# Kernel optimization log

Measured on AMD Instinct MI355X. Metric: run time of the kernel, lower is better.

The kernel has to match this reference:

```python
import jax, jax.numpy as jnp
from jax import lax
import numpy as np

# ChannelMamba (bimamba_type='v2') from Wave-MambaAD VSSBlock.
# Dims: b=4, d_model=256 (channel dim of u), h=w=64 -> l=h*w=4096=dim,
# expand=1 -> d_inner=256, d_state=16, dt_rank=ceil(256/16)=16.
B_, DM, H_, W_ = 4, 256, 64, 64
L_ = H_ * W_            # == init arg `dim` (LayerNorm + depthwise-conv channels)
DI = DM                 # d_inner = expand * d_model
N_ = 16                 # d_state
R_ = 16                 # dt_rank


def setup_inputs() -> dict:
    key = jax.random.key(0)
    ks = jax.random.split(key, 12)
    s = 0.05
    # dt_proj bias init exactly as in the module: inv-softplus of dt in [1e-3, 1e-1]
    rs = np.random.RandomState(0)
    dt = np.exp(rs.rand(DI) * (np.log(0.1) - np.log(0.001)) + np.log(0.001))
    dt = np.clip(dt, 1e-4, None)
    inv_dt = dt + np.log1p(-np.exp(-dt))
    A_log = jnp.log(jnp.tile(jnp.arange(1, N_ + 1, dtype=jnp.float32), (DI, 1)))
    return {
        "u": jax.random.normal(ks[0], (B_, DM, H_, W_), jnp.float32),
        "in_proj_w": jax.random.normal(ks[1], (2 * DI, DM), jnp.float32) * s,
        "conv_w": jax.random.normal(ks[2], (L_, 1, 3, 3), jnp.float32) * s,  # depthwise, groups=L_
        "conv_b": jnp.zeros((L_,), jnp.float32),
        "x_proj_w": jax.random.normal(ks[3], (R_ + 2 * N_, DI), jnp.float32) * s,
        "dt_proj_w": jax.random.normal(ks[4], (DI, R_), jnp.float32) * (R_ ** -0.5),
        "dt_bias": jnp.asarray(inv_dt, jnp.float32),
        "A_log": A_log,
        "D": jnp.ones((DI,), jnp.float32),
        "x_proj_b_w": jax.random.normal(ks[5], (R_ + 2 * N_, DI), jnp.float32) * s,
        "dt_proj_b_w": jax.random.normal(ks[6], (DI, R_), jnp.float32) * (R_ ** -0.5),
        "A_b_log": A_log,
        "D_b": jnp.ones((DI,), jnp.float32),
        "ln_w": jnp.ones((L_,), jnp.float32),
        "ln_b": jnp.zeros((L_,), jnp.float32),
        "ln1_w": jnp.ones((L_,), jnp.float32),
        "ln1_b": jnp.zeros((L_,), jnp.float32),
    }


def _layernorm(x, w, b, eps=1e-5):
    m = jnp.mean(x, axis=-1, keepdims=True)
    v = jnp.mean(jnp.square(x - m), axis=-1, keepdims=True)
    return (x - m) * lax.rsqrt(v + eps) * w + b


def _selective_scan(u, delta, A, Bm, Cm, D, z, delta_bias):
    # u, delta, z: (b,d,l); A: (d,n); Bm, Cm: (b,n,l); D, delta_bias: (d,)
    delta = jax.nn.softplus(delta + delta_bias[None, :, None])
    dT = jnp.transpose(delta, (2, 0, 1))  # (l,b,d)
    uT = jnp.transpose(u, (2, 0, 1))      # (l,b,d)
    BT = jnp.transpose(Bm, (2, 0, 1))     # (l,b,n)
    CT = jnp.transpose(Cm, (2, 0, 1))     # (l,b,n)

    def step(hcar, inp):
        d_t, u_t, B_t, C_t = inp
        dA = jnp.exp(d_t[:, :, None] * A)                       # (b,d,n)
        hcar = hcar * dA + (d_t * u_t)[:, :, None] * B_t[:, None, :]
        y_t = jnp.einsum('bdn,bn->bd', hcar, C_t)
        return hcar, y_t

    h0 = jnp.zeros((u.shape[0], u.shape[1], A.shape[1]), u.dtype)
    _, ys = lax.scan(step, h0, (dT, uT, BT, CT))                 # ys: (l,b,d)
    y = jnp.transpose(ys, (1, 2, 0)) + D[None, :, None] * u      # (b,d,l)
    return y * jax.nn.silu(z)                                    # internal z-gate of selective_scan_fn


def reference(u, in_proj_w, conv_w, conv_b, x_proj_w, dt_proj_w, dt_bias, A_log, D,
              x_proj_b_w, dt_proj_b_w, A_b_log, D_b, ln_w, ln_b, ln1_w, ln1_b):
    b, d, h, w = u.shape
    l = h * w
    r = dt_proj_w.shape[1]
    n = A_log.shape[1]
    u_bld = u.reshape(b, d, l).transpose(0, 2, 1)                # (b,l,d)
    xz = jnp.einsum('ed,bld->bel', in_proj_w, u_bld)             # (b,2*d_inner,l), no bias
    x, z = jnp.split(xz, 2, axis=1)                              # each (b,d_inner,l)

    # depthwise 3x3 conv: channels = l, spatial = (1, d_inner), padding 1 (no activation!)
    xc = x.transpose(0, 2, 1)[:, :, None, :]                     # (b,l,1,d_inner)
    xc = lax.conv_general_dilated(xc, conv_w, (1, 1), ((1, 1), (1, 1)),
                                  feature_group_count=l,
                                  dimension_numbers=('NCHW', 'OIHW', 'NCHW'))
    x = (xc + conv_b[None, :, None, None])[:, :, 0, :].transpose(0, 2, 1)  # (b,d_inner,l)

    def proj(xp_w, dtp_w):
        dbl = jnp.einsum('kd,bdl->bkl', xp_w, x)                 # (b,r+2n,l)
        dt = jnp.einsum('dr,brl->bdl', dtp_w, dbl[:, :r])        # (b,d_inner,l), no bias here
        return dt, dbl[:, r:r + n], dbl[:, r + n:]               # dt, B, C

    A = -jnp.exp(A_log)
    A_b = -jnp.exp(A_b_log)
    dt, Bm, Cm = proj(x_proj_w, dt_proj_w)
    dtb, Bb, Cb = proj(x_proj_b_w, dt_proj_b_w)

    y = _selective_scan(x, dt, A, Bm, Cm, D, z, dt_bias)
    # backward scan: flipped input; NOTE: module uses forward dt_bias and unflipped z here
    yb = _selective_scan(x[:, :, ::-1], dtb, A_b, Bb, Cb, D_b, z, dt_bias)

    out = _layernorm(y, ln_w, ln_b) * jax.nn.silu(z)
    out_b = _layernorm(yb, ln1_w, ln1_b) * jax.nn.silu(z)
    return (out + out_b[:, :, ::-1]).reshape(b, d, h, w)
```

## Files before the change

kernel.cpp:

```cpp
#include <hip/hip_runtime.h>
#include <math.h>

#define BN 4
#define DD 256
#define LL 4096
#define NS 16
#define NCH 128
#define CT 32
#define BROW 20
#define LOG2E 1.4426950408889634f

typedef __bf16 bf16x8 __attribute__((ext_vector_type(8)));
typedef float f32x4 __attribute__((ext_vector_type(4)));

__device__ __forceinline__ float softplus_f(float v) {
  float e = __builtin_amdgcn_exp2f(v * LOG2E);
  float r = 0.69314718056f * __builtin_amdgcn_logf(1.f + e);
  return v > 20.f ? v : r;
}
__device__ __forceinline__ float silu_f(float v) {
  return v / (1.f + __expf(-v));
}
__device__ __forceinline__ f32x4 exp2v(f32x4 a) {
  f32x4 r;
  r[0] = __builtin_amdgcn_exp2f(a[0]);
  r[1] = __builtin_amdgcn_exp2f(a[1]);
  r[2] = __builtin_amdgcn_exp2f(a[2]);
  r[3] = __builtin_amdgcn_exp2f(a[3]);
  return r;
}
__device__ __forceinline__ float quad_reduce(float v) {
  int t = __builtin_amdgcn_mov_dpp(__float_as_int(v), 0xB1, 0xF, 0xF, true);
  v += __int_as_float(t);
  t = __builtin_amdgcn_mov_dpp(__float_as_int(v), 0x4E, 0xF, 0xF, true);
  return v + __int_as_float(t);
}

__global__ __launch_bounds__(256) void k1_mfma(
    const float* __restrict__ W, const float* __restrict__ u,
    float* __restrict__ xpre, float* __restrict__ zb) {
  __shared__ float Af[128 * 36];
  __shared__ float Bf[32 * 68];
  const int l0 = blockIdx.x * 64;
  const int e0 = blockIdx.y * 128;
  const int b  = blockIdx.z;
  const int tid = threadIdx.x;
  const int lane = tid & 63, w = tid >> 6;
  const int m16 = lane & 15, quad = lane >> 4;

  f32x4 acc[2][4];
#pragma unroll
  for (int i = 0; i < 2; ++i)
#pragma unroll
    for (int j = 0; j < 4; ++j) acc[i][j] = (f32x4){0.f, 0.f, 0.f, 0.f};

  const float* Ub = u + (size_t)b * DD * LL;

  for (int k0 = 0; k0 < DD; k0 += 32) {
    if (k0) __syncthreads();
#pragma unroll
    for (int it = 0; it < 4; ++it) {
      int f4 = tid + it * 256;
      int e = f4 >> 3, kq = f4 & 7;
      *(float4*)&Af[e * 36 + kq * 4] =
          *(const float4*)(W + (size_t)(e0 + e) * DD + k0 + kq * 4);
    }
#pragma unroll
    for (int it = 0; it < 2; ++it) {
      int f4 = tid + it * 256;
      int kk = f4 >> 4, lq = f4 & 15;
      *(float4*)&Bf[kk * 68 + lq * 4] =
          *(const float4*)(Ub + (size_t)(k0 + kk) * LL + l0 + lq * 4);
    }
    __syncthreads();
    bf16x8 afr[2], bfr[4];
#pragma unroll
    for (int te = 0; te < 2; ++te) {
      const float* src = &Af[(w * 32 + te * 16 + m16) * 36 + quad * 8];
      bf16x8 t;
#pragma unroll
      for (int j = 0; j < 8; ++j) t[j] = (__bf16)src[j];
      afr[te] = t;
    }
#pragma unroll
    for (int tl = 0; tl < 4; ++tl) {
      bf16x8 t;
#pragma unroll
      for (int j = 0; j < 8; ++j) t[j] = (__bf16)Bf[(quad * 8 + j) * 68 + tl * 16 + m16];
      bfr[tl] = t;
    }
#pragma unroll
    for (int te = 0; te < 2; ++te)
#pragma unroll
      for (int tl = 0; tl < 4; ++tl)
        acc[te][tl] = __builtin_amdgcn_mfma_f32_16x16x32_bf16(afr[te], bfr[tl], acc[te][tl], 0, 0, 0);
  }

#pragma unroll
  for (int te = 0; te < 2; ++te) {
#pragma unroll
    for (int tl = 0; tl < 4; ++tl) {
      int col = l0 + tl * 16 + m16;
#pragma unroll
      for (int r = 0; r < 4; ++r) {
        int e = e0 + w * 32 + te * 16 + quad * 4 + r;
        float v = acc[te][tl][r];
        if (e < DD) xpre[((size_t)b * DD + e) * LL + col] = v;
        else        zb[((size_t)b * DD + (e - DD)) * LL + col] = v;
      }
    }
  }
}

__global__ __launch_bounds__(256) void k2_conv(
    const float* __restrict__ xpre, const float* __restrict__ cw,
    const float* __restrict__ cb, float* __restrict__ xo) {
  const int bd = blockIdx.x;
  const int d = bd & 255;
  const size_t row = (size_t)bd * LL;
  const float* r1 = xpre + row;
  const bool has0 = d > 0, has2 = d < DD - 1;
  for (int j = threadIdx.x; j < LL; j += 256) {
    float w0 = cw[j * 9 + 3], w1 = cw[j * 9 + 4], w2 = cw[j * 9 + 5];
    float v = cb[j] + r1[j] * w1;
    if (has0) v += r1[j - LL] * w0;
    if (has2) v += r1[j + LL] * w2;
    xo[row + j] = v;
  }
}

__global__ __launch_bounds__(256) void k3_xproj(
    const float* __restrict__ xc,
    const float* __restrict__ xpw, const float* __restrict__ xpwB,
    float* __restrict__ dtr, float* __restrict__ gB, float* __restrict__ gC) {
  const int tid = threadIdx.x;
  const int l   = blockIdx.x * 256 + tid;
  const int b   = blockIdx.y;
  const int zz  = blockIdx.z;
  const int dir = zz >> 3, rg = zz & 7;
  const int rbase = rg * 6;
  const float* W = (dir ? xpwB : xpw) + (size_t)rbase * DD;
  const float* xcol = xc + (size_t)b * DD * LL + l;

  float acc[6] = {0.f, 0.f, 0.f, 0.f, 0.f, 0.f};

#pragma unroll 8
  for (int d = 0; d < DD; ++d) {
    float xv = xcol[(size_t)d * LL];
#pragma unroll
    for (int i = 0; i < 6; ++i) acc[i] += W[i * DD + d] * xv;
  }

  const size_t ob = ((size_t)dir * BN + b);
#pragma unroll
  for (int i = 0; i < 6; ++i) {
    int r = rbase + i;
    if (r < 16)
      dtr[(ob * 16 + r) * LL + l] = acc[i];
    else if (r < 32)
      gB[(ob * NS + (r - 16)) * LL + l] = acc[i];
    else
      gC[(ob * NS + (r - 32)) * LL + l] = acc[i];
  }
}

__global__ __launch_bounds__(256) void k3b_dtproj(
    const float* __restrict__ dtr,
    const float* __restrict__ dtw, const float* __restrict__ dtwB,
    const float* __restrict__ dtb,
    float* __restrict__ gdelta) {
  const int tid = threadIdx.x;
  const int l   = blockIdx.x * 256 + tid;
  const int b   = blockIdx.y & 3;
  const int dir = blockIdx.y >> 2;
  const int d0  = blockIdx.z * 16;
  const size_t ob = ((size_t)dir * BN + b);
  const float* dw = (dir ? dtwB : dtw);

  float tr[16];
#pragma unroll
  for (int r = 0; r < 16; ++r) tr[r] = dtr[(ob * 16 + r) * LL + l];

#pragma unroll
  for (int d = d0; d < d0 + 16; ++d) {
    float acc = dtb[d];
#pragma unroll
    for (int r = 0; r < 16; ++r) acc += dw[d * 16 + r] * tr[r];
    gdelta[(ob * DD + d) * LL + l] = softplus_f(acc);
  }
}

__global__ __launch_bounds__(256) void k4_scanA(
    const float* __restrict__ gdelta, const float* __restrict__ x,
    const float* __restrict__ gB,
    const float* __restrict__ Alog, const float* __restrict__ AlogB,
    float* __restrict__ Sbuf, float* __restrict__ qbuf) {
  __shared__ __align__(16) float sB[CT * BROW];
  const int s = blockIdx.x;
  const int d0 = blockIdx.y * 64;
  const int dir = blockIdx.z >> 2, b = blockIdx.z & 3;
  const int t0 = s * CT;
  const int tid = threadIdx.x;
  const size_t ob = (size_t)dir * BN + b;

  {
    const int t = tid & 31, n8 = tid >> 5;
#pragma unroll
    for (int p = 0; p < 2; ++p) {
      int n = n8 + p * 8;
      sB[t * BROW + n] = gB[(ob * NS + n) * LL + t0 + t];
    }
  }
  __syncthreads();

  const int dq = tid >> 2, sub = tid & 3, n0 = sub * 4;
  const int d = d0 + dq;
  f32x4 Al = *(const f32x4*)((dir ? AlogB : Alog) + d * NS + n0);
  f32x4 An2;
  An2[0] = -__expf(Al[0]) * LOG2E;
  An2[1] = -__expf(Al[1]) * LOG2E;
  An2[2] = -__expf(Al[2]) * LOG2E;
  An2[3] = -__expf(Al[3]) * LOG2E;

  const float* dlrow = gdelta + (ob * DD + d) * LL + t0;
  const float* xrow  = x + ((size_t)b * DD + d) * LL;

  f32x4 h = (f32x4){0.f, 0.f, 0.f, 0.f};
  float S = 0.f;

  for (int jb = 0; jb < CT; jb += 4) {
    f32x4 dl4 = *(const f32x4*)(dlrow + jb);
    f32x4 x4;
    if (dir == 0) {
      x4 = *(const f32x4*)(xrow + t0 + jb);
    } else {
      f32x4 t = *(const f32x4*)(xrow + (LL - 4 - t0 - jb));
      x4 = (f32x4){t[3], t[2], t[1], t[0]};
    }
#pragma unroll
    for (int q = 0; q < 4; ++q) {
      int t = jb + q;
      f32x4 Bv = *(const f32x4*)&sB[t * BROW + n0];
      float dl = dl4[q];
      float dlx = dl * x4[q];
      f32x4 e = exp2v(dl * An2);
      h = h * e + dlx * Bv;
      S += dl;
    }
  }

  if (sub == 0) Sbuf[(ob * DD + d) * (size_t)NCH + s] = S;
  const size_t pidx = ((ob * DD + d) * (size_t)NCH + s) * NS + n0;
  *(f32x4*)(qbuf + pidx) = h;
}

__global__ __launch_bounds__(64) void k5_mid(
    const float* __restrict__ Sbuf,
    const float* __restrict__ Alog, const float* __restrict__ AlogB,
    float* __restrict__ qbuf) {
  int id = blockIdx.x * 64 + threadIdx.x;
  int n = id & 15;
  int d = (id >> 4) & 255;
  int rb = id >> 12;
  int dir = rb >> 2;
  float An2 = -__expf((dir ? AlogB : Alog)[d * NS + n]) * LOG2E;
  size_t base = (((size_t)rb * DD + d) * NCH) * NS + n;
  size_t sbase = ((size_t)rb * DD + d) * NCH;
  float h = 0.f;
  for (int s0 = 0; s0 < NCH; s0 += 8) {
    float Sv[8], qv[8];
#pragma unroll
    for (int k = 0; k < 8; ++k) {
      Sv[k] = Sbuf[sbase + s0 + k];
      qv[k] = qbuf[base + (size_t)(s0 + k) * NS];
    }
#pragma unroll
    for (int k = 0; k < 8; ++k) {
      size_t idx = base + (size_t)(s0 + k) * NS;
      qbuf[idx] = h;
      h = h * __builtin_amdgcn_exp2f(An2 * Sv[k]) + qv[k];
    }
  }
}

__global__ __launch_bounds__(256) void k6_scanC(
    const float* __restrict__ gdelta, const float* __restrict__ x,
    const float* __restrict__ gB, const float* __restrict__ gC,
    const float* __restrict__ zb,
    const float* __restrict__ Alog, const float* __restrict__ AlogB,
    const float* __restrict__ Dvec, const float* __restrict__ DvecB,
    const float* __restrict__ hstart,
    float* __restrict__ y, float* __restrict__ yb) {
  __shared__ __align__(16) float sB[CT * BROW];
  __shared__ __align__(16) float sC[CT * BROW];
  const int s = blockIdx.x;
  const int d0 = blockIdx.y * 64;
  const int dir = blockIdx.z >> 2, b = blockIdx.z & 3;
  const int t0 = s * CT;
  const int tid = threadIdx.x;
  const size_t ob = (size_t)dir * BN + b;

  {
    const int t = tid & 31, n8 = tid >> 5;
#pragma unroll
    for (int p = 0; p < 2; ++p) {
      int n = n8 + p * 8;
      sB[t * BROW + n] = gB[(ob * NS + n) * LL + t0 + t];
      sC[t * BROW + n] = gC[(ob * NS + n) * LL + t0 + t];
    }
  }
  __syncthreads();

  const int dq = tid >> 2, sub = tid & 3, n0 = sub * 4;
  const int d = d0 + dq;
  f32x4 Al = *(const f32x4*)((dir ? AlogB : Alog) + d * NS + n0);
  f32x4 An2;
  An2[0] = -__expf(Al[0]) * LOG2E;
  An2[1] = -__expf(Al[1]) * LOG2E;
  An2[2] = -__expf(Al[2]) * LOG2E;
  An2[3] = -__expf(Al[3]) * LOG2E;
  const float Dd = (dir ? DvecB : Dvec)[d];

  const size_t pidx = ((ob * DD + d) * (size_t)NCH + s) * NS + n0;
  f32x4 h = *(const f32x4*)(hstart + pidx);

  const float* dlrow = gdelta + (ob * DD + d) * LL + t0;
  const float* xrow  = x + ((size_t)b * DD + d) * LL;

  float yreg[8], xreg[8];

  for (int jb = 0; jb < CT; jb += 8) {
    f32x4 dlA = *(const f32x4*)(dlrow + jb);
    f32x4 dlB = *(const f32x4*)(dlrow + jb + 4);
    f32x4 xA, xB;
    if (dir == 0) {
      xA = *(const f32x4*)(xrow + t0 + jb);
      xB = *(const f32x4*)(xrow + t0 + jb + 4);
    } else {
      f32x4 ta = *(const f32x4*)(xrow + (LL - 4 - t0 - jb));
      f32x4 tb = *(const f32x4*)(xrow + (LL - 4 - t0 - (jb + 4)));
      xA = (f32x4){ta[3], ta[2], ta[1], ta[0]};
      xB = (f32x4){tb[3], tb[2], tb[1], tb[0]};
    }
    const bool own = (sub == (jb >> 3));
#pragma unroll
    for (int tl = 0; tl < 8; ++tl) {
      float dl = tl < 4 ? dlA[tl & 3] : dlB[tl & 3];
      float xv = tl < 4 ? xA[tl & 3] : xB[tl & 3];
      int t = jb + tl;
      f32x4 Bv = *(const f32x4*)&sB[t * BROW + n0];
      f32x4 Cv = *(const f32x4*)&sC[t * BROW + n0];
      float dlx = dl * xv;
      f32x4 e = exp2v(dl * An2);
      h = h * e + dlx * Bv;
      f32x4 yc = h * Cv;
      float part = (yc[0] + yc[1]) + (yc[2] + yc[3]);
      float sum = quad_reduce(part);
      yreg[tl] = own ? sum : yreg[tl];
      xreg[tl] = own ? xv : xreg[tl];
    }
  }

  const size_t rbase = ((size_t)b * DD + d) * LL + t0 + sub * 8;
  f32x4 z0 = *(const f32x4*)(zb + rbase);
  f32x4 z1 = *(const f32x4*)(zb + rbase + 4);
  float* dst = (dir ? yb : y) + rbase;
  f32x4 o0, o1;
#pragma unroll
  for (int i = 0; i < 4; ++i) {
    o0[i] = (yreg[i] + Dd * xreg[i]) * silu_f(z0[i]);
    o1[i] = (yreg[i + 4] + Dd * xreg[i + 4]) * silu_f(z1[i]);
  }
  *(f32x4*)dst = o0;
  *(f32x4*)(dst + 4) = o1;
}

__global__ __launch_bounds__(256) void k7_final(
    const float* __restrict__ y, const float* __restrict__ yb,
    const float* __restrict__ zb,
    const float* __restrict__ lnw, const float* __restrict__ lnb,
    const float* __restrict__ ln1w, const float* __restrict__ ln1b,
    float* __restrict__ out) {
  __shared__ float sy[LL];
  __shared__ float syb[LL];
  __shared__ float rsum[4][4];
  const int row = blockIdx.x;
  const int tid = threadIdx.x;
  const size_t base = (size_t)row * LL;
  float s1y = 0.f, s2y = 0.f, s1b = 0.f, s2b = 0.f;
  for (int j = tid * 4; j < LL; j += 1024) {
    float4 v = *(const float4*)(y + base + j);
    *(float4*)&sy[j] = v;
    s1y += v.x + v.y + v.z + v.w;
    s2y += v.x * v.x + v.y * v.y + v.z * v.z + v.w * v.w;
    float4 w = *(const float4*)(yb + base + j);
    *(float4*)&syb[j] = w;
    s1b += w.x + w.y + w.z + w.w;
    s2b += w.x * w.x + w.y * w.y + w.z * w.z + w.w * w.w;
  }
#pragma unroll
  for (int m = 1; m < 64; m <<= 1) {
    s1y += __shfl_xor(s1y, m); s2y += __shfl_xor(s2y, m);
    s1b += __shfl_xor(s1b, m); s2b += __shfl_xor(s2b, m);
  }
  int wv = tid >> 6;
  if ((tid & 63) == 0) { rsum[wv][0] = s1y; rsum[wv][1] = s2y; rsum[wv][2] = s1b; rsum[wv][3] = s2b; }
  __syncthreads();
  float t1y = rsum[0][0] + rsum[1][0] + rsum[2][0] + rsum[3][0];
  float t2y = rsum[0][1] + rsum[1][1] + rsum[2][1] + rsum[3][1];
  float t1b = rsum[0][2] + rsum[1][2] + rsum[2][2] + rsum[3][2];
  float t2b = rsum[0][3] + rsum[1][3] + rsum[2][3] + rsum[3][3];
  const float inv = 1.f / (float)LL;
  float mY = t1y * inv; float vY = t2y * inv - mY * mY; float rY = rsqrtf(vY + 1e-5f);
  float mB = t1b * inv; float vB = t2b * inv - mB * mB; float rB = rsqrtf(vB + 1e-5f);
  for (int j = tid; j < LL; j += 256) {
    int jr = LL - 1 - j;
    float a  = (sy[j]  - mY) * rY * lnw[j]   + lnb[j];
    float g1 = silu_f(zb[base + j]);
    float bv = (syb[jr] - mB) * rB * ln1w[jr] + ln1b[jr];
    float g2 = silu_f(zb[base + jr]);
    out[base + j] = a * g1 + bv * g2;
  }
}

extern "C" void kernel_launch(void* const* d_in, const int* in_sizes, int n_in,
                              void* d_out, int out_size, void* d_ws, size_t ws_size,
                              hipStream_t stream) {
  const float* u     = (const float*)d_in[0];
  const float* inw   = (const float*)d_in[1];
  const float* cw    = (const float*)d_in[2];
  const float* cb    = (const float*)d_in[3];
  const float* xpw   = (const float*)d_in[4];
  const float* dtw   = (const float*)d_in[5];
  const float* dtb   = (const float*)d_in[6];
  const float* Alog  = (const float*)d_in[7];
  const float* Dv    = (const float*)d_in[8];
  const float* xpwB  = (const float*)d_in[9];
  const float* dtwB  = (const float*)d_in[10];
  const float* AlogB = (const float*)d_in[11];
  const float* DvB   = (const float*)d_in[12];
  const float* lnw   = (const float*)d_in[13];
  const float* lnb   = (const float*)d_in[14];
  const float* ln1w  = (const float*)d_in[15];
  const float* ln1b  = (const float*)d_in[16];
  float* out = (float*)d_out;

  float* ws = (float*)d_ws;
  const size_t SZ = (size_t)BN * DD * LL;
  float* xpre   = ws;
  float* zb     = ws + SZ;
  float* xc     = ws + 2 * SZ;
  float* gdelta = ws + 3 * SZ;
  float* gB     = ws + 5 * SZ;
  float* gC     = gB + SZ / 8;
  float* Pregion= gC + SZ / 8;
  float* qbuf   = Pregion + SZ;
  float* Sbuf   = Pregion;
  float* ybuf   = xpre;
  float* ybbuf  = Pregion;
  float* dtr    = Pregion;

  k1_mfma<<<dim3(64, 4, 4), 256, 0, stream>>>(inw, u, xpre, zb);
  k2_conv<<<1024, 256, 0, stream>>>(xpre, cw, cb, xc);
  k3_xproj<<<dim3(16, 4, 16), 256, 0, stream>>>(xc, xpw, xpwB, dtr, gB, gC);
  k3b_dtproj<<<dim3(16, 8, 16), 256, 0, stream>>>(dtr, dtw, dtwB, dtb, gdelta);
  k4_scanA<<<dim3(NCH - 1, 4, 8), 256, 0, stream>>>(gdelta, xc, gB, Alog, AlogB, Sbuf, qbuf);
  k5_mid<<<512, 64, 0, stream>>>(Sbuf, Alog, AlogB, qbuf);
  k6_scanC<<<dim3(NCH, 4, 8), 256, 0, stream>>>(gdelta, xc, gB, gC, zb, Alog, AlogB,
                                                Dv, DvB, qbuf, ybuf, ybbuf);
  k7_final<<<1024, 256, 0, stream>>>(ybuf, ybbuf, zb, lnw, lnb, ln1w, ln1b, out);
}
```

Baseline: 259.5 us.

## Fuse both x_proj directions, prefetch scan inputs before barrier, retune mid-scan kernel

k3_xproj now computes both scan directions in one thread, so each xc column is loaded once instead of twice and the grid is halved. In k4 and k6 the delta and x values for the whole chunk are loaded into registers before the shared-memory barrier, overlapping global latency with the B/C staging; k6 also reloads x at the end instead of carrying xreg. k5_mid uses 256-thread blocks and precomputes its exp2 factors ahead of the serial recurrence. These changes raise register pressure, which may lower occupancy.

```diff
diff --git a/kernel.cpp b/kernel.cpp
--- a/kernel.cpp
+++ b/kernel.cpp
@@ -136,31 +136,39 @@
   const int tid = threadIdx.x;
   const int l   = blockIdx.x * 256 + tid;
   const int b   = blockIdx.y;
-  const int zz  = blockIdx.z;
-  const int dir = zz >> 3, rg = zz & 7;
+  const int rg  = blockIdx.z;
   const int rbase = rg * 6;
-  const float* W = (dir ? xpwB : xpw) + (size_t)rbase * DD;
+  const float* W0 = xpw  + (size_t)rbase * DD;
+  const float* W1 = xpwB + (size_t)rbase * DD;
   const float* xcol = xc + (size_t)b * DD * LL + l;
 
-  float acc[6] = {0.f, 0.f, 0.f, 0.f, 0.f, 0.f};
+  float a0[6] = {0.f, 0.f, 0.f, 0.f, 0.f, 0.f};
+  float a1[6] = {0.f, 0.f, 0.f, 0.f, 0.f, 0.f};
 
 #pragma unroll 8
   for (int d = 0; d < DD; ++d) {
     float xv = xcol[(size_t)d * LL];
 #pragma unroll
-    for (int i = 0; i < 6; ++i) acc[i] += W[i * DD + d] * xv;
-  }
-
-  const size_t ob = ((size_t)dir * BN + b);
-#pragma unroll
-  for (int i = 0; i < 6; ++i) {
-    int r = rbase + i;
-    if (r < 16)
-      dtr[(ob * 16 + r) * LL + l] = acc[i];
-    else if (r < 32)
-      gB[(ob * NS + (r - 16)) * LL + l] = acc[i];
-    else
-      gC[(ob * NS + (r - 32)) * LL + l] = acc[i];
+    for (int i = 0; i < 6; ++i) {
+      a0[i] += W0[i * DD + d] * xv;
+      a1[i] += W1[i * DD + d] * xv;
+    }
+  }
+
+#pragma unroll
+  for (int dir = 0; dir < 2; ++dir) {
+    const size_t ob = (size_t)dir * BN + b;
+    const float* acc = dir ? a1 : a0;
+#pragma unroll
+    for (int i = 0; i < 6; ++i) {
+      int r = rbase + i;
+      if (r < 16)
+        dtr[(ob * 16 + r) * LL + l] = acc[i];
+      else if (r < 32)
+        gB[(ob * NS + (r - 16)) * LL + l] = acc[i];
+      else
+        gC[(ob * NS + (r - 32)) * LL + l] = acc[i];
+    }
   }
 }
 
@@ -211,10 +219,24 @@
       sB[t * BROW + n] = gB[(ob * NS + n) * LL + t0 + t];
     }
   }
-  __syncthreads();
 
   const int dq = tid >> 2, sub = tid & 3, n0 = sub * 4;
   const int d = d0 + dq;
+  const float* dlrow = gdelta + (ob * DD + d) * LL + t0;
+  const float* xrow  = x + ((size_t)b * DD + d) * LL;
+
+  f32x4 dlv[8], xv[8];
+#pragma unroll
+  for (int i = 0; i < 8; ++i) {
+    dlv[i] = *(const f32x4*)(dlrow + i * 4);
+    if (dir == 0) {
+      xv[i] = *(const f32x4*)(xrow + t0 + i * 4);
+    } else {
+      f32x4 t = *(const f32x4*)(xrow + (LL - 4 - t0 - i * 4));
+      xv[i] = (f32x4){t[3], t[2], t[1], t[0]};
+    }
+  }
+
   f32x4 Al = *(const f32x4*)((dir ? AlogB : Alog) + d * NS + n0);
   f32x4 An2;
   An2[0] = -__expf(Al[0]) * LOG2E;
@@ -222,31 +244,19 @@
   An2[2] = -__expf(Al[2]) * LOG2E;
   An2[3] = -__expf(Al[3]) * LOG2E;
 
-  const float* dlrow = gdelta + (ob * DD + d) * LL + t0;
-  const float* xrow  = x + ((size_t)b * DD + d) * LL;
+  __syncthreads();
 
   f32x4 h = (f32x4){0.f, 0.f, 0.f, 0.f};
   float S = 0.f;
 
-  for (int jb = 0; jb < CT; jb += 4) {
-    f32x4 dl4 = *(const f32x4*)(dlrow + jb);
-    f32x4 x4;
-    if (dir == 0) {
-      x4 = *(const f32x4*)(xrow + t0 + jb);
-    } else {
-      f32x4 t = *(const f32x4*)(xrow + (LL - 4 - t0 - jb));
-      x4 = (f32x4){t[3], t[2], t[1], t[0]};
-    }
-#pragma unroll
-    for (int q = 0; q < 4; ++q) {
-      int t = jb + q;
-      f32x4 Bv = *(const f32x4*)&sB[t * BROW + n0];
-      float dl = dl4[q];
-      float dlx = dl * x4[q];
-      f32x4 e = exp2v(dl * An2);
-      h = h * e + dlx * Bv;
-      S += dl;
-    }
+#pragma unroll
+  for (int t = 0; t < CT; ++t) {
+    float dl = dlv[t >> 2][t & 3];
+    float dlx = dl * xv[t >> 2][t & 3];
+    f32x4 Bv = *(const f32x4*)&sB[t * BROW + n0];
+    f32x4 e = exp2v(dl * An2);
+    h = h * e + dlx * Bv;
+    S += dl;
   }
 
   if (sub == 0) Sbuf[(ob * DD + d) * (size_t)NCH + s] = S;
@@ -254,11 +264,11 @@
   *(f32x4*)(qbuf + pidx) = h;
 }
 
-__global__ __launch_bounds__(64) void k5_mid(
+__global__ __launch_bounds__(256) void k5_mid(
     const float* __restrict__ Sbuf,
     const float* __restrict__ Alog, const float* __restrict__ AlogB,
     float* __restrict__ qbuf) {
-  int id = blockIdx.x * 64 + threadIdx.x;
+  int id = blockIdx.x * 256 + threadIdx.x;
   int n = id & 15;
   int d = (id >> 4) & 255;
   int rb = id >> 12;
@@ -268,17 +278,19 @@
   size_t sbase = ((size_t)rb * DD + d) * NCH;
   float h = 0.f;
   for (int s0 = 0; s0 < NCH; s0 += 8) {
-    float Sv[8], qv[8];
+    float Sv[8], qv[8], E[8];
 #pragma unroll
     for (int k = 0; k < 8; ++k) {
       Sv[k] = Sbuf[sbase + s0 + k];
       qv[k] = qbuf[base + (size_t)(s0 + k) * NS];
     }
 #pragma unroll
+    for (int k = 0; k < 8; ++k) E[k] = __builtin_amdgcn_exp2f(An2 * Sv[k]);
+#pragma unroll
     for (int k = 0; k < 8; ++k) {
       size_t idx = base + (size_t)(s0 + k) * NS;
       qbuf[idx] = h;
-      h = h * __builtin_amdgcn_exp2f(An2 * Sv[k]) + qv[k];
+      h = h * E[k] + qv[k];
     }
   }
 }
@@ -309,10 +321,26 @@
       sC[t * BROW + n] = gC[(ob * NS + n) * LL + t0 + t];
     }
   }
-  __syncthreads();
 
   const int dq = tid >> 2, sub = tid & 3, n0 = sub * 4;
   const int d = d0 + dq;
+  const float* dlrow = gdelta + (ob * DD + d) * LL + t0;
+  const float* xrow  = x + ((size_t)b * DD + d) * LL;
+
+  f32x4 dlv[8], xv[8];
+#pragma unroll
+  for (int i = 0; i < 8; ++i) {
+    dlv[i] = *(const f32x4*)(dlrow + i * 4);
+    if (dir == 0) {
+      xv[i] = *(const f32x4*)(xrow + t0 + i * 4);
+    } else {
+      f32x4 t = *(const f32x4*)(xrow + (LL - 4 - t0 - i * 4));
+      xv[i] = (f32x4){t[3], t[2], t[1], t[0]};
+    }
+  }
+  const size_t pidx = ((ob * DD + d) * (size_t)NCH + s) * NS + n0;
+  f32x4 h = *(const f32x4*)(hstart + pidx);
+
   f32x4 Al = *(const f32x4*)((dir ? AlogB : Alog) + d * NS + n0);
   f32x4 An2;
   An2[0] = -__expf(Al[0]) * LOG2E;
@@ -321,55 +349,48 @@
   An2[3] = -__expf(Al[3]) * LOG2E;
   const float Dd = (dir ? DvecB : Dvec)[d];
 
-  const size_t pidx = ((ob * DD + d) * (size_t)NCH + s) * NS + n0;
-  f32x4 h = *(const f32x4*)(hstart + pidx);
-
-  const float* dlrow = gdelta + (ob * DD + d) * LL + t0;
-  const float* xrow  = x + ((size_t)b * DD + d) * LL;
-
-  float yreg[8], xreg[8];
-
+  __syncthreads();
+
+  float yreg[8];
+#pragma unroll
   for (int jb = 0; jb < CT; jb += 8) {
-    f32x4 dlA = *(const f32x4*)(dlrow + jb);
-    f32x4 dlB = *(const f32x4*)(dlrow + jb + 4);
-    f32x4 xA, xB;
-    if (dir == 0) {
-      xA = *(const f32x4*)(xrow + t0 + jb);
-      xB = *(const f32x4*)(xrow + t0 + jb + 4);
-    } else {
-      f32x4 ta = *(const f32x4*)(xrow + (LL - 4 - t0 - jb));
-      f32x4 tb = *(const f32x4*)(xrow + (LL - 4 - t0 - (jb + 4)));
-      xA = (f32x4){ta[3], ta[2], ta[1], ta[0]};
-      xB = (f32x4){tb[3], tb[2], tb[1], tb[0]};
-    }
     const bool own = (sub == (jb >> 3));
 #pragma unroll
     for (int tl = 0; tl < 8; ++tl) {
-      float dl = tl < 4 ? dlA[tl & 3] : dlB[tl & 3];
-      float xv = tl < 4 ? xA[tl & 3] : xB[tl & 3];
       int t = jb + tl;
+      float dl = dlv[t >> 2][t & 3];
+      float dlx = dl * xv[t >> 2][t & 3];
       f32x4 Bv = *(const f32x4*)&sB[t * BROW + n0];
       f32x4 Cv = *(const f32x4*)&sC[t * BROW + n0];
-      float dlx = dl * xv;
       f32x4 e = exp2v(dl * An2);
       h = h * e + dlx * Bv;
       f32x4 yc = h * Cv;
       float part = (yc[0] + yc[1]) + (yc[2] + yc[3]);
       float sum = quad_reduce(part);
       yreg[tl] = own ? sum : yreg[tl];
-      xreg[tl] = own ? xv : xreg[tl];
-    }
-  }
-
-  const size_t rbase = ((size_t)b * DD + d) * LL + t0 + sub * 8;
+    }
+  }
+
+  const int s8 = sub * 8;
+  const size_t rbase = ((size_t)b * DD + d) * LL + t0 + s8;
   f32x4 z0 = *(const f32x4*)(zb + rbase);
   f32x4 z1 = *(const f32x4*)(zb + rbase + 4);
+  f32x4 xo0, xo1;
+  if (dir == 0) {
+    xo0 = *(const f32x4*)(xrow + t0 + s8);
+    xo1 = *(const f32x4*)(xrow + t0 + s8 + 4);
+  } else {
+    f32x4 ta = *(const f32x4*)(xrow + (LL - 4 - t0 - s8));
+    f32x4 tb = *(const f32x4*)(xrow + (LL - 4 - t0 - (s8 + 4)));
+    xo0 = (f32x4){ta[3], ta[2], ta[1], ta[0]};
+    xo1 = (f32x4){tb[3], tb[2], tb[1], tb[0]};
+  }
   float* dst = (dir ? yb : y) + rbase;
   f32x4 o0, o1;
 #pragma unroll
   for (int i = 0; i < 4; ++i) {
-    o0[i] = (yreg[i] + Dd * xreg[i]) * silu_f(z0[i]);
-    o1[i] = (yreg[i + 4] + Dd * xreg[i + 4]) * silu_f(z1[i]);
+    o0[i] = (yreg[i] + Dd * xo0[i]) * silu_f(z0[i]);
+    o1[i] = (yreg[i + 4] + Dd * xo1[i]) * silu_f(z1[i]);
   }
   *(f32x4*)dst = o0;
   *(f32x4*)(dst + 4) = o1;
@@ -462,10 +483,10 @@
 
   k1_mfma<<<dim3(64, 4, 4), 256, 0, stream>>>(inw, u, xpre, zb);
   k2_conv<<<1024, 256, 0, stream>>>(xpre, cw, cb, xc);
-  k3_xproj<<<dim3(16, 4, 16), 256, 0, stream>>>(xc, xpw, xpwB, dtr, gB, gC);
+  k3_xproj<<<dim3(16, 4, 8), 256, 0, stream>>>(xc, xpw, xpwB, dtr, gB, gC);
   k3b_dtproj<<<dim3(16, 8, 16), 256, 0, stream>>>(dtr, dtw, dtwB, dtb, gdelta);
   k4_scanA<<<dim3(NCH - 1, 4, 8), 256, 0, stream>>>(gdelta, xc, gB, Alog, AlogB, Sbuf, qbuf);
-  k5_mid<<<512, 64, 0, stream>>>(Sbuf, Alog, AlogB, qbuf);
+  k5_mid<<<128, 256, 0, stream>>>(Sbuf, Alog, AlogB, qbuf);
   k6_scanC<<<dim3(NCH, 4, 8), 256, 0, stream>>>(gdelta, xc, gB, gC, zb, Alog, AlogB,
                                                 Dv, DvB, qbuf, ybuf, ybbuf);
   k7_final<<<1024, 256, 0, stream>>>(ybuf, ybbuf, zb, lnw, lnb, ln1w, ln1b, out);
```

Measured after the change: 276.8 us. 1.07x slower.
